# Optimization experiments

Hardware: AMD Instinct MI355X
Metric: run time of the kernel (lower is better)

The kernel has to match this reference:

```python
import jax, jax.numpy as jnp
import numpy as np

B, C, H, W = 8, 64, 32, 32
NEG = 256
TEMP = 2.0
FACTOR = 0.8
EPS = 1e-8


def setup_inputs() -> dict:
    key = jax.random.key(0)
    k1, k2, k3, k4 = jax.random.split(key, 4)
    views_1 = jax.random.normal(k1, (B, C, H, W), dtype=jnp.float32)
    views_2 = jax.random.normal(k2, (B, C, H, W), dtype=jnp.float32)
    img = jax.random.uniform(k3, (1, 3, H, W), dtype=jnp.float32)
    neg_idx = jax.random.randint(k4, (B, 2, H * W, NEG), 0, H, dtype=jnp.int32)
    return {"views_1": views_1, "views_2": views_2, "img": img, "neg_idx": neg_idx}


def _forward(views_1, views_2, img, neg_idx):
    hw = H * W
    height = jnp.arange(hw) // W
    width = jnp.arange(hw) % W
    coords = jnp.stack([height, width]).astype(jnp.float32)  # [2, hw]
    img0 = img[0]  # [3, H, W]; original uses img[0] for EVERY batch element
    euc_norm = jnp.sqrt(jnp.asarray((H - 1) ** 2 + (W - 1) ** 2, jnp.float32))
    sqrt3 = jnp.sqrt(jnp.asarray(3.0, jnp.float32))

    center = img0[:, height, width]  # [3, hw]

    def per_sample(z1, z2, nidx):
        # nidx: [2, hw, neg]
        nf = nidx.astype(jnp.float32)
        # torch.norm with no dim => scalar Frobenius norm over [2, neg] per pixel
        d = coords[:, :, None] - nf  # [2, hw, neg]
        euc = jnp.sqrt(jnp.sum(d * d, axis=(0, 2))) / euc_norm  # [hw]
        negs = img0[:, nidx[0], nidx[1]]  # [3, hw, neg]
        rd = center[:, :, None] - negs
        rgb = jnp.sqrt(jnp.sum(rd * rd, axis=(0, 2))) / sqrt3  # [hw]
        weight = euc * FACTOR + rgb * (1.0 - FACTOR)  # [hw], constant across neg

        z1v = z1.reshape(C, hw)  # [c, hw]
        pn = z2[:, nidx[0], nidx[1]]  # [c, hw, neg]
        dot = jnp.einsum('cp,cpn->pn', z1v, pn)  # [hw, neg]
        z1sq = jnp.sum(z1v * z1v, axis=0)  # [hw]
        z1n = jnp.sqrt(z1sq)
        pnn = jnp.sqrt(jnp.sum(pn * pn, axis=0))  # [hw, neg]
        cos = dot / jnp.maximum(z1n[:, None] * pnn, EPS)  # [hw, neg]
        cos0 = z1sq / jnp.maximum(z1sq, EPS)  # [hw] (self-similarity ~ 1)

        sim_neg = jnp.minimum(jnp.abs(cos * weight[:, None]), 1.0)  # [hw, neg]
        sim0 = jnp.minimum(jnp.abs(cos0), 1.0)  # [hw]
        sim = jnp.concatenate(
            [jnp.mean(sim0)[None], jnp.mean(sim_neg, axis=0) / TEMP]
        )  # [neg+1]

        # BCELoss with target = [1, 0, ..., 0]; torch clamps log terms at -100
        logp = jnp.maximum(jnp.log(sim[0]), -100.0)
        log1m = jnp.maximum(jnp.log1p(-sim[1:]), -100.0)
        bce = -(logp + jnp.sum(log1m)) / (NEG + 1)
        return bce, sim

    bce, sims = jax.vmap(per_sample)(views_1, views_2, neg_idx)
    loss = jnp.mean(bce)
    sim_all = jnp.sum(sims, axis=0)
    return (loss, sim_all[0] / B, jnp.sum(sim_all[1:]) / NEG * TEMP / B)


def reference(views_1, views_2, img, neg_idx):
    return _forward(views_1, views_2, img, neg_idx)
```

## Files before the change

### kernel.cpp

```cpp
#include <hip/hip_runtime.h>
#include <math.h>

#define BB 8
#define CC 64
#define HH 32
#define WW 32
#define HW 1024
#define NEGN 256
#define TEMP 2.0f
#define FACTOR 0.8f
#define EPSF 1e-8f
#define PT 8

__global__ __launch_bounds__(256) void contrastive_fused(
    const float* __restrict__ z1,
    const float* __restrict__ z2,
    const float* __restrict__ img,
    const int*   __restrict__ nidx,
    float* __restrict__ accSim,
    float* __restrict__ accSim0)
{
    __shared__ float As_s[CC * PT];
    __shared__ float Dt_s[PT * HW];
    __shared__ float normq_s[HW];
    __shared__ float imgs[3 * HW];
    __shared__ float simpart[PT * NEGN];
    __shared__ float z1sqs[PT];

    const int t  = threadIdx.x;
    const int b  = blockIdx.x >> 7;
    const int p0 = (blockIdx.x & 127) * PT;

    const int lane32 = t & 31;
    const int pp_b   = t >> 5;
    const int p_b    = p0 + pp_b;

    int rr[8], cc_[8];
    const size_t nbase = ((size_t)(b * 2) * HW + p_b) * NEGN;
    #pragma unroll
    for (int j = 0; j < 8; ++j) {
        rr[j]  = nidx[nbase + lane32 + 32 * j];
        cc_[j] = nidx[nbase + (size_t)HW * NEGN + lane32 + 32 * j];
    }

    for (int i = t; i < CC * PT; i += 256) {
        const int c = i >> 3, pp = i & 7;
        As_s[i] = z1[((size_t)(b * CC + c)) * HW + p0 + pp];
    }
    for (int i = t; i < 3 * HW; i += 256) imgs[i] = img[i];
    __syncthreads();

    if (t < PT) {
        float s = 0.f;
        #pragma unroll
        for (int c = 0; c < CC; ++c) { const float v = As_s[c * PT + t]; s += v * v; }
        z1sqs[t] = s;
    }

    const float4* __restrict__ z2f4 =
        reinterpret_cast<const float4*>(z2 + (size_t)b * CC * HW);
    float4 acc[PT];
    #pragma unroll
    for (int pp = 0; pp < PT; ++pp) acc[pp] = make_float4(0.f, 0.f, 0.f, 0.f);
    float4 sq = make_float4(0.f, 0.f, 0.f, 0.f);

    #pragma unroll 8
    for (int k = 0; k < CC; ++k) {
        const float4 bv = z2f4[k * (HW / 4) + t];
        sq.x = fmaf(bv.x, bv.x, sq.x);
        sq.y = fmaf(bv.y, bv.y, sq.y);
        sq.z = fmaf(bv.z, bv.z, sq.z);
        sq.w = fmaf(bv.w, bv.w, sq.w);
        const float4 a03 = reinterpret_cast<const float4*>(As_s)[k * 2];
        const float4 a47 = reinterpret_cast<const float4*>(As_s)[k * 2 + 1];
        const float av[8] = {a03.x, a03.y, a03.z, a03.w, a47.x, a47.y, a47.z, a47.w};
        #pragma unroll
        for (int pp = 0; pp < PT; ++pp) {
            acc[pp].x = fmaf(av[pp], bv.x, acc[pp].x);
            acc[pp].y = fmaf(av[pp], bv.y, acc[pp].y);
            acc[pp].z = fmaf(av[pp], bv.z, acc[pp].z);
            acc[pp].w = fmaf(av[pp], bv.w, acc[pp].w);
        }
    }
    float4* Dt4 = reinterpret_cast<float4*>(Dt_s);
    #pragma unroll
    for (int pp = 0; pp < PT; ++pp) Dt4[pp * (HW / 4) + t] = acc[pp];
    reinterpret_cast<float4*>(normq_s)[t] =
        make_float4(sqrtf(sq.x), sqrtf(sq.y), sqrtf(sq.z), sqrtf(sq.w));
    __syncthreads();

    const float z1sq = z1sqs[pp_b];
    const float z1n  = sqrtf(z1sq);
    const float cen0 = imgs[p_b], cen1 = imgs[HW + p_b], cen2 = imgs[2 * HW + p_b];
    const float hp = (float)(p_b >> 5), wp = (float)(p_b & 31);

    float se = 0.f, sr = 0.f;
    float cosv[8];
    #pragma unroll
    for (int j = 0; j < 8; ++j) {
        const int q = rr[j] * WW + cc_[j];
        const float dh = hp - (float)rr[j], dw = wp - (float)cc_[j];
        se += dh * dh + dw * dw;
        const float d0 = cen0 - imgs[q];
        const float d1 = cen1 - imgs[HW + q];
        const float d2 = cen2 - imgs[2 * HW + q];
        sr += d0 * d0 + d1 * d1 + d2 * d2;
        const float dot = Dt_s[pp_b * HW + q];
        const float pnn = normq_s[q];
        cosv[j] = dot / fmaxf(z1n * pnn, EPSF);
    }
    #pragma unroll
    for (int off = 16; off; off >>= 1) {
        se += __shfl_xor(se, off);
        sr += __shfl_xor(sr, off);
    }
    const float euc_norm = sqrtf((float)((HH - 1) * (HH - 1) + (WW - 1) * (WW - 1)));
    const float weight = sqrtf(se) / euc_norm * FACTOR +
                         sqrtf(sr) / sqrtf(3.0f) * (1.0f - FACTOR);
    #pragma unroll
    for (int j = 0; j < 8; ++j)
        simpart[pp_b * NEGN + lane32 + 32 * j] = fminf(fabsf(cosv[j] * weight), 1.0f);
    __syncthreads();

    float s = 0.f;
    #pragma unroll
    for (int pp = 0; pp < PT; ++pp) s += simpart[pp * NEGN + t];
    atomicAdd(accSim + b * NEGN + t, s);

    if (t < PT) {
        const float c0 = z1sq / fmaxf(z1sq, EPSF);
        float s0 = fminf(fabsf(c0), 1.0f);
        #pragma unroll
        for (int off = 4; off; off >>= 1) s0 += __shfl_xor(s0, off);
        if (t == 0) atomicAdd(accSim0 + b, s0);
    }
}

__global__ __launch_bounds__(256) void finalize(
    const float* __restrict__ accSim,
    const float* __restrict__ accSim0,
    float* __restrict__ out)
{
    const int t = threadIdx.x;
    float ssum = 0.f, lsum = 0.f;
    #pragma unroll
    for (int b = 0; b < BB; ++b) {
        const float s = accSim[b * NEGN + t] * (1.0f / HW) * (1.0f / TEMP);
        ssum += s;
        lsum += fmaxf(log1pf(-s), -100.0f);
    }
    __shared__ float rs[4], rl[4];
    #pragma unroll
    for (int off = 32; off; off >>= 1) {
        ssum += __shfl_down(ssum, off);
        lsum += __shfl_down(lsum, off);
    }
    if ((t & 63) == 0) { rs[t >> 6] = ssum; rl[t >> 6] = lsum; }
    __syncthreads();

    if (t == 0) {
        const float S = rs[0] + rs[1] + rs[2] + rs[3];
        const float L = rl[0] + rl[1] + rl[2] + rl[3];
        float logpsum = 0.f, sim0sum = 0.f;
        #pragma unroll
        for (int b = 0; b < BB; ++b) {
            const float s0 = accSim0[b] * (1.0f / HW);
            sim0sum += s0;
            logpsum += fmaxf(logf(s0), -100.0f);
        }
        out[0] = -(logpsum + L) / ((float)(NEGN + 1) * (float)BB);
        out[1] = sim0sum / (float)BB;
        out[2] = S / (float)NEGN * TEMP / (float)BB;
    }
}

extern "C" void kernel_launch(void* const* d_in, const int* in_sizes, int n_in,
                              void* d_out, int out_size, void* d_ws, size_t ws_size,
                              hipStream_t stream) {
    const float* v1   = (const float*)d_in[0];
    const float* v2   = (const float*)d_in[1];
    const float* img  = (const float*)d_in[2];
    const int*   nidx = (const int*)  d_in[3];

    float* accSim  = (float*)d_ws;
    float* accSim0 = accSim + BB * NEGN;

    hipMemsetAsync(accSim, 0, (BB * NEGN + BB) * sizeof(float), stream);

    contrastive_fused<<<BB * (HW / PT), 256, 0, stream>>>(
        v1, v2, img, nidx, accSim, accSim0);
    finalize<<<1, 256, 0, stream>>>(accSim, accSim0, (float*)d_out);
}
```

Baseline: 105.3 us.

## Drop shared image copy and remap threads to negatives, removing simpart buffer

Each block no longer copies the whole 3x1024 image into LDS. It loads only the 8 center pixels and gathers neighbor colors straight from global memory, which should hit in cache. Threads now own one negative index across all 8 pixels, so the per-pixel sums are reduced block-wide through a small shared array and the simpart buffer and its pass go away. LDS use drops to raise occupancy, with a launch-bounds hint of 4 blocks. The cost is scattered global gathers and more shuffle and reduction work per pixel.

```diff
diff --git a/kernel.cpp b/kernel.cpp
--- a/kernel.cpp
+++ b/kernel.cpp
@@ -12,7 +12,7 @@
 #define EPSF 1e-8f
 #define PT 8
 
-__global__ __launch_bounds__(256) void contrastive_fused(
+__global__ __launch_bounds__(256, 4) void contrastive_fused(
     const float* __restrict__ z1,
     const float* __restrict__ z2,
     const float* __restrict__ img,
@@ -23,31 +23,19 @@
     __shared__ float As_s[CC * PT];
     __shared__ float Dt_s[PT * HW];
     __shared__ float normq_s[HW];
-    __shared__ float imgs[3 * HW];
-    __shared__ float simpart[PT * NEGN];
+    __shared__ float cen_s[3 * PT];
     __shared__ float z1sqs[PT];
+    __shared__ float wred_s[PT][4][2];
 
     const int t  = threadIdx.x;
     const int b  = blockIdx.x >> 7;
     const int p0 = (blockIdx.x & 127) * PT;
 
-    const int lane32 = t & 31;
-    const int pp_b   = t >> 5;
-    const int p_b    = p0 + pp_b;
-
-    int rr[8], cc_[8];
-    const size_t nbase = ((size_t)(b * 2) * HW + p_b) * NEGN;
-    #pragma unroll
-    for (int j = 0; j < 8; ++j) {
-        rr[j]  = nidx[nbase + lane32 + 32 * j];
-        cc_[j] = nidx[nbase + (size_t)HW * NEGN + lane32 + 32 * j];
-    }
-
     for (int i = t; i < CC * PT; i += 256) {
         const int c = i >> 3, pp = i & 7;
         As_s[i] = z1[((size_t)(b * CC + c)) * HW + p0 + pp];
     }
-    for (int i = t; i < 3 * HW; i += 256) imgs[i] = img[i];
+    if (t < 3 * PT) cen_s[t] = img[(t >> 3) * HW + p0 + (t & 7)];
     __syncthreads();
 
     if (t < PT) {
@@ -87,52 +75,73 @@
     for (int pp = 0; pp < PT; ++pp) Dt4[pp * (HW / 4) + t] = acc[pp];
     reinterpret_cast<float4*>(normq_s)[t] =
         make_float4(sqrtf(sq.x), sqrtf(sq.y), sqrtf(sq.z), sqrtf(sq.w));
-    __syncthreads();
-
-    const float z1sq = z1sqs[pp_b];
-    const float z1n  = sqrtf(z1sq);
-    const float cen0 = imgs[p_b], cen1 = imgs[HW + p_b], cen2 = imgs[2 * HW + p_b];
-    const float hp = (float)(p_b >> 5), wp = (float)(p_b & 31);
-
-    float se = 0.f, sr = 0.f;
-    float cosv[8];
-    #pragma unroll
-    for (int j = 0; j < 8; ++j) {
-        const int q = rr[j] * WW + cc_[j];
-        const float dh = hp - (float)rr[j], dw = wp - (float)cc_[j];
-        se += dh * dh + dw * dw;
-        const float d0 = cen0 - imgs[q];
-        const float d1 = cen1 - imgs[HW + q];
-        const float d2 = cen2 - imgs[2 * HW + q];
-        sr += d0 * d0 + d1 * d1 + d2 * d2;
-        const float dot = Dt_s[pp_b * HW + q];
-        const float pnn = normq_s[q];
-        cosv[j] = dot / fmaxf(z1n * pnn, EPSF);
-    }
-    #pragma unroll
-    for (int off = 16; off; off >>= 1) {
-        se += __shfl_xor(se, off);
-        sr += __shfl_xor(sr, off);
-    }
+
+    int rr[PT], cc_[PT];
+    const size_t nb0 = ((size_t)(b * 2) * HW + p0) * NEGN;
+    #pragma unroll
+    for (int pp = 0; pp < PT; ++pp) {
+        rr[pp]  = nidx[nb0 + (size_t)pp * NEGN + t];
+        cc_[pp] = nidx[nb0 + (size_t)HW * NEGN + (size_t)pp * NEGN + t];
+    }
+    __syncthreads();
+
+    float se[PT], sr[PT];
+    #pragma unroll
+    for (int pp = 0; pp < PT; ++pp) {
+        const int q  = rr[pp] * WW + cc_[pp];
+        const float hp = (float)((p0 + pp) >> 5);
+        const float wp = (float)((p0 + pp) & 31);
+        const float dh = hp - (float)rr[pp], dw = wp - (float)cc_[pp];
+        se[pp] = dh * dh + dw * dw;
+        const float d0 = cen_s[pp]          - img[q];
+        const float d1 = cen_s[PT + pp]     - img[HW + q];
+        const float d2 = cen_s[2 * PT + pp] - img[2 * HW + q];
+        sr[pp] = d0 * d0 + d1 * d1 + d2 * d2;
+    }
+    #pragma unroll
+    for (int off = 32; off; off >>= 1) {
+        #pragma unroll
+        for (int pp = 0; pp < PT; ++pp) {
+            se[pp] += __shfl_xor(se[pp], off);
+            sr[pp] += __shfl_xor(sr[pp], off);
+        }
+    }
+    if ((t & 63) == 0) {
+        const int wv = t >> 6;
+        #pragma unroll
+        for (int pp = 0; pp < PT; ++pp) {
+            wred_s[pp][wv][0] = se[pp];
+            wred_s[pp][wv][1] = sr[pp];
+        }
+    }
+    __syncthreads();
+
     const float euc_norm = sqrtf((float)((HH - 1) * (HH - 1) + (WW - 1) * (WW - 1)));
-    const float weight = sqrtf(se) / euc_norm * FACTOR +
-                         sqrtf(sr) / sqrtf(3.0f) * (1.0f - FACTOR);
-    #pragma unroll
-    for (int j = 0; j < 8; ++j)
-        simpart[pp_b * NEGN + lane32 + 32 * j] = fminf(fabsf(cosv[j] * weight), 1.0f);
-    __syncthreads();
-
+    const float wE = FACTOR / euc_norm;
+    const float wR = (1.0f - FACTOR) / sqrtf(3.0f);
     float s = 0.f;
     #pragma unroll
-    for (int pp = 0; pp < PT; ++pp) s += simpart[pp * NEGN + t];
+    for (int pp = 0; pp < PT; ++pp) {
+        const float SE = wred_s[pp][0][0] + wred_s[pp][1][0] +
+                         wred_s[pp][2][0] + wred_s[pp][3][0];
+        const float SR = wred_s[pp][0][1] + wred_s[pp][1][1] +
+                         wred_s[pp][2][1] + wred_s[pp][3][1];
+        const float weight = sqrtf(SE) * wE + sqrtf(SR) * wR;
+        const int q = rr[pp] * WW + cc_[pp];
+        const float dot = Dt_s[pp * HW + q];
+        const float cosv = dot / fmaxf(sqrtf(z1sqs[pp]) * normq_s[q], EPSF);
+        s += fminf(fabsf(cosv * weight), 1.0f);
+    }
     atomicAdd(accSim + b * NEGN + t, s);
 
-    if (t < PT) {
-        const float c0 = z1sq / fmaxf(z1sq, EPSF);
-        float s0 = fminf(fabsf(c0), 1.0f);
-        #pragma unroll
-        for (int off = 4; off; off >>= 1) s0 += __shfl_xor(s0, off);
-        if (t == 0) atomicAdd(accSim0 + b, s0);
+    if (t == 0) {
+        float s0 = 0.f;
+        #pragma unroll
+        for (int pp = 0; pp < PT; ++pp) {
+            const float c0 = z1sqs[pp] / fmaxf(z1sqs[pp], EPSF);
+            s0 += fminf(fabsf(c0), 1.0f);
+        }
+        atomicAdd(accSim0 + b, s0);
     }
 }
 
```

Result: slower. 112.6 us (+7.0%).

## Cut shared memory, prefetch z2 in registers, gather image from global

Applied to the files above, without the earlier changes.

Drops the full-image shared copy and reads the image gathers straight from global memory, keeping only the 8 center pixels in shared. Reuses the Dt_s buffer for the per-pixel similarity partials, with an added barrier, and sets launch bounds to 4 blocks per SM to raise occupancy. The z2 loads in the GEMM loop are software-prefetched 4 steps ahead, and the neighbor-index loads are moved after the GEMM to shorten register live ranges. The trade-off is scattered global gathers for the image in place of LDS reads, plus higher register pressure from the prefetch buffer.

```diff
diff --git a/kernel.cpp b/kernel.cpp
--- a/kernel.cpp
+++ b/kernel.cpp
@@ -12,7 +12,7 @@
 #define EPSF 1e-8f
 #define PT 8
 
-__global__ __launch_bounds__(256) void contrastive_fused(
+__global__ __launch_bounds__(256, 4) void contrastive_fused(
     const float* __restrict__ z1,
     const float* __restrict__ z2,
     const float* __restrict__ img,
@@ -23,8 +23,7 @@
     __shared__ float As_s[CC * PT];
     __shared__ float Dt_s[PT * HW];
     __shared__ float normq_s[HW];
-    __shared__ float imgs[3 * HW];
-    __shared__ float simpart[PT * NEGN];
+    __shared__ float cen_s[3 * PT];
     __shared__ float z1sqs[PT];
 
     const int t  = threadIdx.x;
@@ -35,19 +34,11 @@
     const int pp_b   = t >> 5;
     const int p_b    = p0 + pp_b;
 
-    int rr[8], cc_[8];
-    const size_t nbase = ((size_t)(b * 2) * HW + p_b) * NEGN;
-    #pragma unroll
-    for (int j = 0; j < 8; ++j) {
-        rr[j]  = nidx[nbase + lane32 + 32 * j];
-        cc_[j] = nidx[nbase + (size_t)HW * NEGN + lane32 + 32 * j];
-    }
-
     for (int i = t; i < CC * PT; i += 256) {
         const int c = i >> 3, pp = i & 7;
         As_s[i] = z1[((size_t)(b * CC + c)) * HW + p0 + pp];
     }
-    for (int i = t; i < 3 * HW; i += 256) imgs[i] = img[i];
+    if (t < 3 * PT) cen_s[t] = img[(t >> 3) * HW + p0 + (t & 7)];
     __syncthreads();
 
     if (t < PT) {
@@ -59,55 +50,94 @@
 
     const float4* __restrict__ z2f4 =
         reinterpret_cast<const float4*>(z2 + (size_t)b * CC * HW);
+
     float4 acc[PT];
     #pragma unroll
     for (int pp = 0; pp < PT; ++pp) acc[pp] = make_float4(0.f, 0.f, 0.f, 0.f);
     float4 sq = make_float4(0.f, 0.f, 0.f, 0.f);
 
-    #pragma unroll 8
-    for (int k = 0; k < CC; ++k) {
-        const float4 bv = z2f4[k * (HW / 4) + t];
-        sq.x = fmaf(bv.x, bv.x, sq.x);
-        sq.y = fmaf(bv.y, bv.y, sq.y);
-        sq.z = fmaf(bv.z, bv.z, sq.z);
-        sq.w = fmaf(bv.w, bv.w, sq.w);
-        const float4 a03 = reinterpret_cast<const float4*>(As_s)[k * 2];
-        const float4 a47 = reinterpret_cast<const float4*>(As_s)[k * 2 + 1];
-        const float av[8] = {a03.x, a03.y, a03.z, a03.w, a47.x, a47.y, a47.z, a47.w};
-        #pragma unroll
-        for (int pp = 0; pp < PT; ++pp) {
-            acc[pp].x = fmaf(av[pp], bv.x, acc[pp].x);
-            acc[pp].y = fmaf(av[pp], bv.y, acc[pp].y);
-            acc[pp].z = fmaf(av[pp], bv.z, acc[pp].z);
-            acc[pp].w = fmaf(av[pp], bv.w, acc[pp].w);
-        }
-    }
+    float4 pf[4];
+    #pragma unroll
+    for (int i = 0; i < 4; ++i) pf[i] = z2f4[i * (HW / 4) + t];
+
+#define GEMM_STEP(kk, bv)                                                      \
+    {                                                                          \
+        sq.x = fmaf((bv).x, (bv).x, sq.x);                                     \
+        sq.y = fmaf((bv).y, (bv).y, sq.y);                                     \
+        sq.z = fmaf((bv).z, (bv).z, sq.z);                                     \
+        sq.w = fmaf((bv).w, (bv).w, sq.w);                                     \
+        const float4 a03 = reinterpret_cast<const float4*>(As_s)[(kk) * 2];    \
+        const float4 a47 = reinterpret_cast<const float4*>(As_s)[(kk) * 2 + 1];\
+        const float av[8] = {a03.x, a03.y, a03.z, a03.w,                       \
+                             a47.x, a47.y, a47.z, a47.w};                      \
+        _Pragma("unroll")                                                      \
+        for (int pp = 0; pp < PT; ++pp) {                                      \
+            acc[pp].x = fmaf(av[pp], (bv).x, acc[pp].x);                       \
+            acc[pp].y = fmaf(av[pp], (bv).y, acc[pp].y);                       \
+            acc[pp].z = fmaf(av[pp], (bv).z, acc[pp].z);                       \
+            acc[pp].w = fmaf(av[pp], (bv).w, acc[pp].w);                       \
+        }                                                                      \
+    }
+
+    #pragma unroll 4
+    for (int k = 0; k < CC - 4; ++k) {
+        const float4 bv = pf[k & 3];
+        pf[k & 3] = z2f4[(k + 4) * (HW / 4) + t];
+        GEMM_STEP(k, bv);
+    }
+    #pragma unroll
+    for (int k = CC - 4; k < CC; ++k) {
+        const float4 bv = pf[k & 3];
+        GEMM_STEP(k, bv);
+    }
+#undef GEMM_STEP
+
     float4* Dt4 = reinterpret_cast<float4*>(Dt_s);
     #pragma unroll
     for (int pp = 0; pp < PT; ++pp) Dt4[pp * (HW / 4) + t] = acc[pp];
     reinterpret_cast<float4*>(normq_s)[t] =
         make_float4(sqrtf(sq.x), sqrtf(sq.y), sqrtf(sq.z), sqrtf(sq.w));
+
+    int rr[8], cc_[8];
+    const size_t nbase = ((size_t)(b * 2) * HW + p_b) * NEGN;
+    #pragma unroll
+    for (int j = 0; j < 8; ++j) {
+        rr[j]  = nidx[nbase + lane32 + 32 * j];
+        cc_[j] = nidx[nbase + (size_t)HW * NEGN + lane32 + 32 * j];
+    }
     __syncthreads();
 
     const float z1sq = z1sqs[pp_b];
     const float z1n  = sqrtf(z1sq);
-    const float cen0 = imgs[p_b], cen1 = imgs[HW + p_b], cen2 = imgs[2 * HW + p_b];
+    const float cen0 = cen_s[pp_b], cen1 = cen_s[PT + pp_b], cen2 = cen_s[2 * PT + pp_b];
     const float hp = (float)(p_b >> 5), wp = (float)(p_b & 31);
 
-    float se = 0.f, sr = 0.f;
-    float cosv[8];
-    #pragma unroll
-    for (int j = 0; j < 8; ++j) {
-        const int q = rr[j] * WW + cc_[j];
+    int   qv[8];
+    float g0[8], g1[8], g2[8];
+    #pragma unroll
+    for (int j = 0; j < 8; ++j) {
+        qv[j] = rr[j] * WW + cc_[j];
+        g0[j] = img[qv[j]];
+        g1[j] = img[HW + qv[j]];
+        g2[j] = img[2 * HW + qv[j]];
+    }
+    float dotv[8], pnn[8];
+    #pragma unroll
+    for (int j = 0; j < 8; ++j) {
+        dotv[j] = Dt_s[pp_b * HW + qv[j]];
+        pnn[j]  = normq_s[qv[j]];
+    }
+
+    float se = 0.f, sr = 0.f, cosv[8];
+    #pragma unroll
+    for (int j = 0; j < 8; ++j) {
         const float dh = hp - (float)rr[j], dw = wp - (float)cc_[j];
         se += dh * dh + dw * dw;
-        const float d0 = cen0 - imgs[q];
-        const float d1 = cen1 - imgs[HW + q];
-        const float d2 = cen2 - imgs[2 * HW + q];
+        const float d0 = cen0 - g0[j];
+        const float d1 = cen1 - g1[j];
+        const float d2 = cen2 - g2[j];
         sr += d0 * d0 + d1 * d1 + d2 * d2;
-        const float dot = Dt_s[pp_b * HW + q];
-        const float pnn = normq_s[q];
-        cosv[j] = dot / fmaxf(z1n * pnn, EPSF);
+        cosv[j] = dotv[j] / fmaxf(z1n * pnn[j], EPSF);
     }
     #pragma unroll
     for (int off = 16; off; off >>= 1) {
@@ -117,9 +147,17 @@
     const float euc_norm = sqrtf((float)((HH - 1) * (HH - 1) + (WW - 1) * (WW - 1)));
     const float weight = sqrtf(se) / euc_norm * FACTOR +
                          sqrtf(sr) / sqrtf(3.0f) * (1.0f - FACTOR);
+
+    float simv[8];
     #pragma unroll
     for (int j = 0; j < 8; ++j)
-        simpart[pp_b * NEGN + lane32 + 32 * j] = fminf(fabsf(cosv[j] * weight), 1.0f);
+        simv[j] = fminf(fabsf(cosv[j] * weight), 1.0f);
+
+    __syncthreads();
+    float* simpart = Dt_s;
+    #pragma unroll
+    for (int j = 0; j < 8; ++j)
+        simpart[pp_b * NEGN + lane32 + 32 * j] = simv[j];
     __syncthreads();
 
     float s = 0.f;
@@ -128,7 +166,8 @@
     atomicAdd(accSim + b * NEGN + t, s);
 
     if (t < PT) {
-        const float c0 = z1sq / fmaxf(z1sq, EPSF);
+        const float zz = z1sqs[t];
+        const float c0 = zz / fmaxf(zz, EPSF);
         float s0 = fminf(fabsf(c0), 1.0f);
         #pragma unroll
         for (int off = 4; off; off >>= 1) s0 += __shfl_xor(s0, off);
```

New measurement: 101.9 us. 3.2% less time.
